# Kernel tuning notes

Hardware: AMD Instinct MI355X
Metric: run time of the kernel (lower is better)

Reference implementation:

```python
import jax, jax.numpy as jnp
import numpy as np

# DoG parameters derived from init kwargs: sigma_low=1.0, truncate=4.0
SIGMA_LOW = 1.0
SIGMA_HIGH = 1.6  # sigma_low * 1.6
KSIZE_LOW = 9     # 2*ceil(4.0*1.0)+1
KSIZE_HIGH = 15   # 2*ceil(4.0*1.6)+1


def gaussian_kernel1d(ksize: int, sigma: float) -> jnp.ndarray:
    # Matches kornia's 1D gaussian: centered, normalized to sum 1.
    t = jnp.arange(ksize, dtype=jnp.float32) - (ksize - 1) / 2.0
    g = jnp.exp(-(t * t) / (2.0 * sigma * sigma))
    return g / jnp.sum(g)


def _conv1d_along_axis(x: jnp.ndarray, g: jnp.ndarray, axis: int) -> jnp.ndarray:
    # x: (B, C, D, H, W); depthwise 1D cross-correlation along `axis` with
    # replicate ('edge') boundary handling, as in kornia filter3d(border_type='replicate').
    C = x.shape[1]
    k = g.shape[0]
    pads = [(0, 0)] * 5
    pads[axis] = (k // 2, k // 2)
    xp = jnp.pad(x, pads, mode='edge')
    kshape = [1, 1, 1]
    kshape[axis - 2] = k
    w = jnp.tile(g.reshape(1, 1, *kshape), (C, 1, 1, 1, 1))  # (C,1,kd,kh,kw)
    return jax.lax.conv_general_dilated(
        xp, w, window_strides=(1, 1, 1), padding='VALID',
        dimension_numbers=('NCDHW', 'OIDHW', 'NCDHW'),
        feature_group_count=C)


def gaussian_blur3d(x: jnp.ndarray, sigma: float, ksize: int) -> jnp.ndarray:
    # The 3D kernel is an outer product of normalized 1D gaussians, so the
    # dense 3D convolution is exactly equal to three separable 1D passes.
    g = gaussian_kernel1d(ksize, sigma)
    for ax in (2, 3, 4):
        x = _conv1d_along_axis(x, g, ax)
    return x


def setup_inputs() -> dict:
    key = jax.random.key(0)
    x = jax.random.normal(key, (2, 1, 160, 160, 160), dtype=jnp.float32)
    return {"x": x}


def reference(x) -> jnp.ndarray:
    low_pass = gaussian_blur3d(x, SIGMA_LOW, KSIZE_LOW)
    high_pass = gaussian_blur3d(x, SIGMA_HIGH, KSIZE_HIGH)
    return low_pass - high_pass
```

## Files before the change

### kernel.cpp

```cpp
#include <hip/hip_runtime.h>
#include <math.h>

#define DIMS 160
#define PLANE (DIMS*DIMS)
#define NB 2
#define RH 7
#define RL 4
#define KH 15
#define KL 9
#define TSX 16
#define TSY 32
#define NTX (DIMS/TSX)
#define NTY (DIMS/TSY)
#define CZ 32
#define NCH (DIMS/CZ)
#define NSTEPS (CZ + 2*RH)
#define YHR (TSY + 2*RH)
#define SR 48
#define SH 50
#define SL 42
#define RAWSZ (YHR*SR)
#define XHSZ (TSX*SH)
#define XLSZ (TSX*SL)
#define NBLK (NTX*NTY*NCH*NB)

struct DoGW { float gl[KL]; float gh[KH]; };

__global__ __launch_bounds__(512, 4)
void dog_v9(const float* __restrict__ X, float* __restrict__ out, DoGW w) {
  __shared__ __align__(16) float sRaw[2][RAWSZ];
  __shared__ __align__(16) float sXh[2][XHSZ];
  __shared__ __align__(16) float sXl[2][XLSZ];

  const int bid = blockIdx.x;
  const int xt = bid % NTX;
  const int yt = (bid / NTX) % NTY;
  const int zc = (bid / (NTX * NTY)) % NCH;
  const int b  = bid / (NTX * NTY * NCH);
  const int x0 = xt * TSX, y0 = yt * TSY, z0 = zc * CZ;
  const float* Xb = X + (size_t)b * DIMS * PLANE;
  const int tid = threadIdx.x;
  const bool xfast = (x0 >= 8) && (x0 + 24 <= DIMS);

  const bool y_on = tid < 256;
  const int cx  = tid & 15;
  const int cy0 = 2 * ((tid >> 4) & 15);
  const int hb = cx * SH + cy0;
  const int lb = cx * SL + cy0;
  float* const obase = out + ((size_t)b * DIMS * PLANE) + (size_t)(y0 + cy0) * DIMS + (x0 + cx);

  const bool x_on = (tid >= 256) && (tid < 256 + YHR * 4);
  const int xu = tid - 256;
  const int xr = xu >> 2, xq = xu & 3;

  const bool l_on = tid >= (512 - YHR * 4);
  const int lu = tid - (512 - YHR * 4);
  const int lrow = lu >> 2, lt = lu & 3;
  const int lyg = min(max(y0 + lrow - RH, 0), DIMS - 1);
  const int lxb = x0 - 8 + 4 * lt;

  float4 vA, vB;

  auto loadP = [&](int s) {
    const int zsrc = min(max(z0 - RH + s, 0), DIMS - 1);
    const float* rowp = Xb + ((size_t)zsrc * DIMS + lyg) * DIMS;
    if (xfast) {
      vA = *(const float4*)(rowp + lxb);
      vB = *(const float4*)(rowp + lxb + 16);
    } else {
      vA.x = rowp[min(max(lxb + 0, 0), DIMS - 1)];
      vA.y = rowp[min(max(lxb + 1, 0), DIMS - 1)];
      vA.z = rowp[min(max(lxb + 2, 0), DIMS - 1)];
      vA.w = rowp[min(max(lxb + 3, 0), DIMS - 1)];
      vB.x = rowp[min(max(lxb + 16, 0), DIMS - 1)];
      vB.y = rowp[min(max(lxb + 17, 0), DIMS - 1)];
      vB.z = rowp[min(max(lxb + 18, 0), DIMS - 1)];
      vB.w = rowp[min(max(lxb + 19, 0), DIMS - 1)];
    }
  };
  auto stageP = [&](int buf) {
    float* p = &sRaw[buf][lrow * SR + 4 * lt];
    *(float4*)(p) = vA;
    *(float4*)(p + 16) = vB;
  };

  float accH0[KH], accH1[KH], accL0[KL + 3], accL1[KL + 3];
  #pragma unroll
  for (int i = 0; i < KH; ++i) { accH0[i] = 0.f; accH1[i] = 0.f; }
  #pragma unroll
  for (int i = 0; i < KL + 3; ++i) { accL0[i] = 0.f; accL1[i] = 0.f; }

  auto consumeQ = [&](int q) {
    const int qb = q & 1;
    float f[16], g[10];
    #pragma unroll
    for (int j = 0; j < 8; ++j) {
      float2 t = *(const float2*)&sXh[qb][hb + 2 * j];
      f[2 * j] = t.x; f[2 * j + 1] = t.y;
    }
    #pragma unroll
    for (int j = 0; j < 5; ++j) {
      float2 t = *(const float2*)&sXl[qb][lb + 2 * j];
      g[2 * j] = t.x; g[2 * j + 1] = t.y;
    }
    float ph0 = 0.f, ph1 = 0.f, pl0 = 0.f, pl1 = 0.f;
    #pragma unroll
    for (int j = 0; j < KH; ++j) {
      ph0 = fmaf(w.gh[j], f[j], ph0);
      ph1 = fmaf(w.gh[j], f[j + 1], ph1);
    }
    #pragma unroll
    for (int j = 0; j < KL; ++j) {
      pl0 = fmaf(w.gl[j], g[j], pl0);
      pl1 = fmaf(w.gl[j], g[j + 1], pl1);
    }
    #pragma unroll
    for (int i = 0; i < KH; ++i) {
      accH0[i] = fmaf(w.gh[KH - 1 - i], ph0, accH0[i]);
      accH1[i] = fmaf(w.gh[KH - 1 - i], ph1, accH1[i]);
    }
    #pragma unroll
    for (int i = 3; i < KL + 3; ++i) {
      accL0[i] = fmaf(w.gl[KL + 2 - i], pl0, accL0[i]);
      accL1[i] = fmaf(w.gl[KL + 2 - i], pl1, accL1[i]);
    }
    if (q >= 2 * RH) {
      float* op = obase + (size_t)(z0 + q - 2 * RH) * PLANE;
      op[0]    = accL0[0] - accH0[0];
      op[DIMS] = accL1[0] - accH1[0];
    }
    #pragma unroll
    for (int i = 0; i < KH - 1; ++i) { accH0[i] = accH0[i + 1]; accH1[i] = accH1[i + 1]; }
    accH0[KH - 1] = 0.f; accH1[KH - 1] = 0.f;
    #pragma unroll
    for (int i = 0; i < KL + 2; ++i) { accL0[i] = accL0[i + 1]; accL1[i] = accL1[i + 1]; }
    accL0[KL + 2] = 0.f; accL1[KL + 2] = 0.f;
  };

  auto xconvP = [&](int cur) {
    const float* p = &sRaw[cur][xr * SR + 4 * xq];
    float v[20];
    #pragma unroll
    for (int j = 0; j < 5; ++j) {
      float4 t = *(const float4*)(p + 4 * j);
      v[4 * j] = t.x; v[4 * j + 1] = t.y; v[4 * j + 2] = t.z; v[4 * j + 3] = t.w;
    }
    #pragma unroll
    for (int c = 0; c < 4; ++c) {
      float a = 0.f;
      #pragma unroll
      for (int k = 0; k < KH; ++k) a = fmaf(w.gh[k], v[c + 1 + k], a);
      sXh[cur][(4 * xq + c) * SH + xr] = a;
    }
    if (xr >= 3 && xr <= 42) {
      #pragma unroll
      for (int c = 0; c < 4; ++c) {
        float a = 0.f;
        #pragma unroll
        for (int k = 0; k < KL; ++k) a = fmaf(w.gl[k], v[c + 4 + k], a);
        sXl[cur][(4 * xq + c) * SL + (xr - 3)] = a;
      }
    }
  };

  if (l_on) { loadP(0); stageP(0); loadP(1); }
  __syncthreads();

  for (int sb = 0; sb < NSTEPS - 1; sb += 5) {
    #pragma unroll
    for (int u = 0; u < 5; ++u) {
      const int s = sb + u;
      const int cur = s & 1;
      if (l_on) {
        if (s + 1 < NSTEPS) stageP(1 - cur);
        if (s + 2 < NSTEPS) loadP(s + 2);
      }
      if (y_on && s >= 1) consumeQ(s - 1);
      if (x_on) xconvP(cur);
      __syncthreads();
    }
  }
  {
    if (y_on) consumeQ(NSTEPS - 2);
    if (x_on) xconvP((NSTEPS - 1) & 1);
    __syncthreads();
    if (y_on) consumeQ(NSTEPS - 1);
  }
}

extern "C" void kernel_launch(void* const* d_in, const int* in_sizes, int n_in,
                              void* d_out, int out_size, void* d_ws, size_t ws_size,
                              hipStream_t stream) {
  const float* X = (const float*)d_in[0];
  float* out = (float*)d_out;

  DoGW w;
  {
    double s = 0.0;
    for (int i = 0; i < KL; ++i) {
      double t = i - (KL - 1) / 2.0;
      double g = exp(-(t * t) / (2.0 * 1.0 * 1.0));
      w.gl[i] = (float)g; s += g;
    }
    for (int i = 0; i < KL; ++i) w.gl[i] = (float)((double)w.gl[i] / s);
    s = 0.0;
    for (int i = 0; i < KH; ++i) {
      double t = i - (KH - 1) / 2.0;
      double g = exp(-(t * t) / (2.0 * 1.6 * 1.6));
      w.gh[i] = (float)g; s += g;
    }
    for (int i = 0; i < KH; ++i) w.gh[i] = (float)((double)w.gh[i] / s);
  }

  dog_v9<<<NBLK, 512, 0, stream>>>(X, out, w);
}
```

Measured before the change: 128.8 us.

## Merge DoG accumulators, halve z-chunk, raise occupancy bound

Folds the high and low z-pass accumulators into one difference register array by negating the high-pass weights, which cuts accumulator registers and the per-step shift work. It halves the z chunk from 32 to 16 to double the number of blocks, and raises the launch_bounds min-blocks hint from 4 to 8 so the compiler targets lower register use. The z-halo overhead grows: each chunk now spends 14 of its 30 steps on halo planes instead of 14 of 46, so more redundant loads and x/y convolutions are done. The step loop is also restructured into a single unrolled loop.

Measured after the change: 238.6 us. +85.2%, slower.

```diff
diff --git a/kernel.cpp b/kernel.cpp
--- a/kernel.cpp
+++ b/kernel.cpp
@@ -12,7 +12,7 @@
 #define TSY 32
 #define NTX (DIMS/TSX)
 #define NTY (DIMS/TSY)
-#define CZ 32
+#define CZ 16
 #define NCH (DIMS/CZ)
 #define NSTEPS (CZ + 2*RH)
 #define YHR (TSY + 2*RH)
@@ -26,8 +26,8 @@
 
 struct DoGW { float gl[KL]; float gh[KH]; };
 
-__global__ __launch_bounds__(512, 4)
-void dog_v9(const float* __restrict__ X, float* __restrict__ out, DoGW w) {
+__global__ __launch_bounds__(512, 8)
+void dog_v10(const float* __restrict__ X, float* __restrict__ out, DoGW w) {
   __shared__ __align__(16) float sRaw[2][RAWSZ];
   __shared__ __align__(16) float sXh[2][XHSZ];
   __shared__ __align__(16) float sXl[2][XLSZ];
@@ -84,11 +84,9 @@
     *(float4*)(p + 16) = vB;
   };
 
-  float accH0[KH], accH1[KH], accL0[KL + 3], accL1[KL + 3];
+  float D0[KH], D1[KH];
   #pragma unroll
-  for (int i = 0; i < KH; ++i) { accH0[i] = 0.f; accH1[i] = 0.f; }
-  #pragma unroll
-  for (int i = 0; i < KL + 3; ++i) { accL0[i] = 0.f; accL1[i] = 0.f; }
+  for (int i = 0; i < KH; ++i) { D0[i] = 0.f; D1[i] = 0.f; }
 
   auto consumeQ = [&](int q) {
     const int qb = q & 1;
@@ -116,25 +114,22 @@
     }
     #pragma unroll
     for (int i = 0; i < KH; ++i) {
-      accH0[i] = fmaf(w.gh[KH - 1 - i], ph0, accH0[i]);
-      accH1[i] = fmaf(w.gh[KH - 1 - i], ph1, accH1[i]);
+      D0[i] = fmaf(-w.gh[KH - 1 - i], ph0, D0[i]);
+      D1[i] = fmaf(-w.gh[KH - 1 - i], ph1, D1[i]);
     }
     #pragma unroll
     for (int i = 3; i < KL + 3; ++i) {
-      accL0[i] = fmaf(w.gl[KL + 2 - i], pl0, accL0[i]);
-      accL1[i] = fmaf(w.gl[KL + 2 - i], pl1, accL1[i]);
+      D0[i] = fmaf(w.gl[KL + 2 - i], pl0, D0[i]);
+      D1[i] = fmaf(w.gl[KL + 2 - i], pl1, D1[i]);
     }
     if (q >= 2 * RH) {
       float* op = obase + (size_t)(z0 + q - 2 * RH) * PLANE;
-      op[0]    = accL0[0] - accH0[0];
-      op[DIMS] = accL1[0] - accH1[0];
-    }
-    #pragma unroll
-    for (int i = 0; i < KH - 1; ++i) { accH0[i] = accH0[i + 1]; accH1[i] = accH1[i + 1]; }
-    accH0[KH - 1] = 0.f; accH1[KH - 1] = 0.f;
-    #pragma unroll
-    for (int i = 0; i < KL + 2; ++i) { accL0[i] = accL0[i + 1]; accL1[i] = accL1[i + 1]; }
-    accL0[KL + 2] = 0.f; accL1[KL + 2] = 0.f;
+      op[0]    = D0[0];
+      op[DIMS] = D1[0];
+    }
+    #pragma unroll
+    for (int i = 0; i < KH - 1; ++i) { D0[i] = D0[i + 1]; D1[i] = D1[i + 1]; }
+    D0[KH - 1] = 0.f; D1[KH - 1] = 0.f;
   };
 
   auto xconvP = [&](int cur) {
@@ -166,26 +161,18 @@
   if (l_on) { loadP(0); stageP(0); loadP(1); }
   __syncthreads();
 
-  for (int sb = 0; sb < NSTEPS - 1; sb += 5) {
-    #pragma unroll
-    for (int u = 0; u < 5; ++u) {
-      const int s = sb + u;
-      const int cur = s & 1;
-      if (l_on) {
-        if (s + 1 < NSTEPS) stageP(1 - cur);
-        if (s + 2 < NSTEPS) loadP(s + 2);
-      }
-      if (y_on && s >= 1) consumeQ(s - 1);
-      if (x_on) xconvP(cur);
-      __syncthreads();
-    }
+  #pragma unroll 5
+  for (int s = 0; s < NSTEPS; ++s) {
+    const int cur = s & 1;
+    if (l_on) {
+      if (s + 1 < NSTEPS) stageP(1 - cur);
+      if (s + 2 < NSTEPS) loadP(s + 2);
+    }
+    if (y_on && s >= 1) consumeQ(s - 1);
+    if (x_on) xconvP(cur);
+    __syncthreads();
   }
-  {
-    if (y_on) consumeQ(NSTEPS - 2);
-    if (x_on) xconvP((NSTEPS - 1) & 1);
-    __syncthreads();
-    if (y_on) consumeQ(NSTEPS - 1);
-  }
+  if (y_on) consumeQ(NSTEPS - 1);
 }
 
 extern "C" void kernel_launch(void* const* d_in, const int* in_sizes, int n_in,
@@ -212,5 +199,5 @@
     for (int i = 0; i < KH; ++i) w.gh[i] = (float)((double)w.gh[i] / s);
   }
 
-  dog_v9<<<NBLK, 512, 0, stream>>>(X, out, w);
+  dog_v10<<<NBLK, 512, 0, stream>>>(X, out, w);
 }
```
